# Performance work log

Hardware: AMD Instinct MI355X
Metric: run time of the kernel (lower is better)

## Reference

```python
import jax, jax.numpy as jnp
import numpy as np

B, N, D, L, NREPEAT = 32, 577, 384, 12, 4
H = 4 * D  # mlp hidden
EPS = 1e-6


def ln(x, w, b):
    mu = jnp.mean(x, axis=-1, keepdims=True)
    var = jnp.mean(jnp.square(x - mu), axis=-1, keepdims=True)
    return (x - mu) * jax.lax.rsqrt(var + EPS) * w + b


def setup_inputs() -> dict:
    key = jax.random.key(0)
    ks = jax.random.split(key, 16)
    s = 0.02
    return {
        "x": jax.random.normal(ks[0], (B, N, D), dtype=jnp.float32),
        "norm1_w": jnp.ones((L, D), jnp.float32),
        "norm1_b": jnp.zeros((L, D), jnp.float32),
        "qkv_w": jax.random.normal(ks[1], (L, 3 * D, D), jnp.float32) * s,
        "qkv_b": jnp.zeros((L, 3 * D), jnp.float32),
        "qn_w": jnp.ones((L, D), jnp.float32),
        "qn_b": jnp.zeros((L, D), jnp.float32),
        "kn_w": jnp.ones((L, D), jnp.float32),
        "kn_b": jnp.zeros((L, D), jnp.float32),
        "an_w": jnp.ones((L, D), jnp.float32),
        "an_b": jnp.zeros((L, D), jnp.float32),
        "proj_w": jax.random.normal(ks[2], (L, D, D), jnp.float32) * s,
        "proj_b": jnp.zeros((L, D), jnp.float32),
        "ls1": jnp.full((L, D), 1e-5, jnp.float32),
        "norm2_w": jnp.ones((L, D), jnp.float32),
        "norm2_b": jnp.zeros((L, D), jnp.float32),
        "fc1_w": jax.random.normal(ks[3], (L, H, D), jnp.float32) * s,
        "fc1_b": jnp.zeros((L, H), jnp.float32),
        "fc2_w": jax.random.normal(ks[4], (L, D, H), jnp.float32) * s,
        "fc2_b": jnp.zeros((L, D), jnp.float32),
        "ls2": jnp.full((L, D), 1e-5, jnp.float32),
    }


def _forward(x, norm1_w, norm1_b, qkv_w, qkv_b, qn_w, qn_b, kn_w, kn_b,
             an_w, an_b, proj_w, proj_b, ls1, norm2_w, norm2_b,
             fc1_w, fc1_b, fc2_w, fc2_b, ls2):
    scale = 1.0 / np.sqrt(D).astype(np.float32)
    x_prime = x
    history = []  # list of [B, 1, D] cls tokens, grows each repeat
    for _ in range(NREPEAT):
        new_cls = x[:, 0:1]
        x = jnp.concatenate([new_cls, x_prime[:, 1:]], axis=1)  # [B, N, D]
        mem = jnp.concatenate([x] + history, axis=1)            # [B, N+t, D]
        for l in range(L):
            res1 = x
            xn = ln(x, norm1_w[l], norm1_b[l])
            # manual qkv split: q from normed x, k/v from UNNORMED mem
            q = xn @ qkv_w[l, :D].T + qkv_b[l, :D]
            k = mem @ qkv_w[l, D:2 * D].T + qkv_b[l, D:2 * D]
            v = mem @ qkv_w[l, 2 * D:].T + qkv_b[l, 2 * D:]
            q = ln(q, qn_w[l], qn_b[l])
            k = ln(k, kn_w[l], kn_b[l])
            # single-head SDPA over full width D
            attn = jax.nn.softmax(jnp.einsum('bqd,bkd->bqk', q, k) * scale, axis=-1)
            prod = jnp.einsum('bqk,bkd->bqd', attn, v)
            prod = ln(prod, an_w[l], an_b[l])
            proj = prod @ proj_w[l].T + proj_b[l]
            x = proj * ls1[l] + res1
            res2 = x
            x2 = ln(x, norm2_w[l], norm2_b[l])
            h = jax.nn.gelu(x2 @ fc1_w[l].T + fc1_b[l], approximate=False)
            x1 = h @ fc2_w[l].T + fc2_b[l]
            x = x1 * ls2[l] + res2
        history.append(new_cls)
    return x


def reference(x, norm1_w, norm1_b, qkv_w, qkv_b, qn_w, qn_b, kn_w, kn_b,
              an_w, an_b, proj_w, proj_b, ls1, norm2_w, norm2_b,
              fc1_w, fc1_b, fc2_w, fc2_b, ls2):
    return _forward(x, norm1_w, norm1_b, qkv_w, qkv_b, qn_w, qn_b, kn_w, kn_b,
                    an_w, an_b, proj_w, proj_b, ls1, norm2_w, norm2_b,
                    fc1_w, fc1_b, fc2_w, fc2_b, ls2)
```

## Files before the change

### kernel.cpp

```cpp
#include <hip/hip_runtime.h>
#include <math.h>

#define BB 32
#define NN 577
#define DD 384
#define HD 1536
#define LL 12
#define MP 640
#define NRPT 4

typedef __attribute__((ext_vector_type(8))) short bf16x8;
typedef __attribute__((ext_vector_type(4))) float f32x4;

__device__ __forceinline__ unsigned short f2bf(float f){
  unsigned u = __builtin_bit_cast(unsigned, f);
  u += 0x7fffu + ((u >> 16) & 1u);
  return (unsigned short)(u >> 16);
}
__device__ __forceinline__ float bf2f(unsigned short s){
  unsigned u = ((unsigned)s) << 16;
  return __builtin_bit_cast(float, u);
}

__device__ __forceinline__ void async16(void* lds, const void* g){
  __builtin_amdgcn_global_load_lds(
      (const __attribute__((address_space(1))) unsigned int*)g,
      (__attribute__((address_space(3))) unsigned int*)lds, 16, 0, 0);
}

__global__ void prep_k(float* __restrict__ x, const float* __restrict__ xp,
                       float* __restrict__ cls_r, const float* __restrict__ cls_hist,
                       unsigned short* __restrict__ mem, int r){
  int i = blockIdx.x * 256 + threadIdx.x;
  if (i >= BB*MP*DD) return;
  int d = i % DD;
  int n = (i / DD) % MP;
  int b = i / (MP*DD);
  float v;
  if (n == 0){ v = x[(size_t)b*NN*DD + d]; cls_r[b*DD + d] = v; }
  else if (n < NN){ v = xp[((size_t)b*NN + n)*DD + d]; x[((size_t)b*NN + n)*DD + d] = v; }
  else if (n < NN + r){ v = cls_hist[(size_t)(n-NN)*BB*DD + b*DD + d]; }
  else v = 0.f;
  mem[i] = f2bf(v);
}

__global__ void castL_k(const float* __restrict__ qkvw, const float* __restrict__ pw,
                        const float* __restrict__ f1w, const float* __restrict__ f2w,
                        unsigned short* __restrict__ wbuf){
  int i = blockIdx.x * 256 + threadIdx.x;
  const int QKV = 3*DD*DD;
  const int PRJ = DD*DD;
  const int F1  = HD*DD;
  const int TOT = QKV + PRJ + 2*F1;
  if (i >= TOT) return;
  float v;
  if (i < QKV) v = qkvw[i];
  else if (i < QKV+PRJ) v = pw[i-QKV];
  else if (i < QKV+PRJ+F1) v = f1w[i-QKV-PRJ];
  else v = f2w[i-QKV-PRJ-F1];
  wbuf[i] = f2bf(v);
}

template<typename T>
__global__ __launch_bounds__(256) void ln4_k(const T* __restrict__ in, const float* __restrict__ w,
                                             const float* __restrict__ bias, unsigned short* __restrict__ out,
                                             int nrows){
  int row = blockIdx.x*4 + (threadIdx.x >> 6);
  if (row >= nrows) return;
  int lane = threadIdx.x & 63;
  const T* p = in + (size_t)row*DD;
  float v[6];
  float s = 0.f;
  #pragma unroll
  for (int i=0;i<6;i++){
    float t;
    if (sizeof(T) == 4) t = (float)p[lane + i*64];
    else t = bf2f((unsigned short)p[lane + i*64]);
    v[i] = t; s += t;
  }
  #pragma unroll
  for (int o=32;o;o>>=1) s += __shfl_xor(s, o, 64);
  float mu = s * (1.f/DD);
  float q = 0.f;
  #pragma unroll
  for (int i=0;i<6;i++){ float t = v[i]-mu; q += t*t; }
  #pragma unroll
  for (int o=32;o;o>>=1) q += __shfl_xor(q, o, 64);
  float rs = rsqrtf(q*(1.f/DD) + 1e-6f);
  unsigned short* po = out + (size_t)row*DD;
  #pragma unroll
  for (int i=0;i<6;i++){
    int c = lane + i*64;
    po[c] = f2bf((v[i]-mu)*rs*w[c] + bias[c]);
  }
}

__global__ __launch_bounds__(256) void lnqk_k(const unsigned short* __restrict__ qraw,
                                              const unsigned short* __restrict__ kraw,
                                              const float* __restrict__ qw, const float* __restrict__ qbias,
                                              const float* __restrict__ kw, const float* __restrict__ kbias,
                                              unsigned short* __restrict__ qo, unsigned short* __restrict__ ko){
  const int QR = BB*NN;
  int row = blockIdx.x*4 + (threadIdx.x >> 6);
  int lane = threadIdx.x & 63;
  bool isq = row < QR;
  const unsigned short* p = isq ? qraw + (size_t)row*DD : kraw + (size_t)(row-QR)*DD;
  const float* w  = isq ? qw : kw;
  const float* bs = isq ? qbias : kbias;
  unsigned short* po = isq ? qo + (size_t)row*DD : ko + (size_t)(row-QR)*DD;
  float scale = isq ? 0.05103103588f : 1.0f;
  float v[6];
  float s = 0.f;
  #pragma unroll
  for (int i=0;i<6;i++){ float t = bf2f(p[lane + i*64]); v[i] = t; s += t; }
  #pragma unroll
  for (int o=32;o;o>>=1) s += __shfl_xor(s, o, 64);
  float mu = s * (1.f/DD);
  float q = 0.f;
  #pragma unroll
  for (int i=0;i<6;i++){ float t = v[i]-mu; q += t*t; }
  #pragma unroll
  for (int o=32;o;o>>=1) q += __shfl_xor(q, o, 64);
  float rs = rsqrtf(q*(1.f/DD) + 1e-6f);
  #pragma unroll
  for (int i=0;i<6;i++){
    int c = lane + i*64;
    po[c] = f2bf(((v[i]-mu)*rs*w[c] + bs[c]) * scale);
  }
}

template<int EPI>
__global__ __launch_bounds__(256) void gemm128(
    const unsigned short* __restrict__ A, int lda, int arows, long sA,
    const unsigned short* __restrict__ B, int ldb, int brows, long sB,
    const float* __restrict__ bias,
    int K, int N,
    float* __restrict__ outF, unsigned short* __restrict__ outB,
    int ldo, int orows, long sO,
    const float* __restrict__ ls){

  __shared__ unsigned short a_sh[2][128*32];
  __shared__ unsigned short b_sh[2][128*32];

  int tid  = threadIdx.x;
  int wave = tid >> 6, lane = tid & 63;
  int lr = lane & 15, kg = lane >> 4;
  int wm = wave >> 1, wn = wave & 1;
  int z = blockIdx.z;
  int row0 = blockIdx.y * 128;
  int col0 = blockIdx.x * 128;

  const unsigned short* Ab = A + (size_t)z*sA;
  const unsigned short* Bb = B + (size_t)z*sB;

  f32x4 zf = {0.f,0.f,0.f,0.f};
  f32x4 acc[4][4];
  #pragma unroll
  for (int i=0;i<4;i++)
    #pragma unroll
    for (int j=0;j<4;j++) acc[i][j] = zf;

  int ra[2], rb[2], kc[2];
  #pragma unroll
  for (int it=0; it<2; it++){
    int c = tid + it*256;
    int r = row0 + (c>>2); if (r > arows-1) r = arows-1;
    ra[it] = r;
    r = col0 + (c>>2); if (r > brows-1) r = brows-1;
    rb[it] = r;
    kc[it] = (c&3)*8;
  }

  for (int k0 = 0; k0 < K; k0 += 64){
    #pragma unroll
    for (int p=0;p<2;p++){
      #pragma unroll
      for (int it=0; it<2; it++){
        unsigned short* la = &a_sh[p][(it*256 + wave*64)*8];
        unsigned short* lb = &b_sh[p][(it*256 + wave*64)*8];
        async16(la, Ab + (size_t)ra[it]*lda + k0 + p*32 + kc[it]);
        async16(lb, Bb + (size_t)rb[it]*ldb + k0 + p*32 + kc[it]);
      }
    }
    __syncthreads();
    #pragma unroll
    for (int p=0;p<2;p++){
      bf16x8 af[4], bfr[4];
      #pragma unroll
      for (int i=0;i<4;i++){
        af[i]  = *(const bf16x8*)&a_sh[p][(wm*64 + i*16 + lr)*32 + kg*8];
        bfr[i] = *(const bf16x8*)&b_sh[p][(wn*64 + i*16 + lr)*32 + kg*8];
      }
      #pragma unroll
      for (int i=0;i<4;i++)
        #pragma unroll
        for (int j=0;j<4;j++)
          acc[i][j] = __builtin_amdgcn_mfma_f32_16x16x32_bf16(af[i], bfr[j], acc[i][j], 0,0,0);
    }
    __syncthreads();
  }

  float* oF = outF ? outF + (size_t)z*sO : nullptr;
  unsigned short* oB = outB ? outB + (size_t)z*sO : nullptr;

  #pragma unroll
  for (int mi=0;mi<4;mi++)
    #pragma unroll
    for (int ni=0;ni<4;ni++)
      #pragma unroll
      for (int r=0;r<4;r++){
        int row = row0 + wm*64 + mi*16 + kg*4 + r;
        int col = col0 + wn*64 + ni*16 + lr;
        if (row >= orows || col >= N) continue;
        float vv = acc[mi][ni][r];
        size_t idx = (size_t)row*ldo + col;
        if (EPI == 0){
          if (bias) vv += bias[col];
          oB[idx] = f2bf(vv);
        } else if (EPI == 1){
          vv += bias[row];
          oB[idx] = f2bf(vv);
        } else if (EPI == 2){
          vv += bias[col];
          oF[idx] = vv*ls[col] + oF[idx];
        } else {
          vv += bias[col];
          float g = 0.5f*vv*(1.f + erff(vv*0.70710678118f));
          oB[idx] = f2bf(g);
        }
      }
}

__global__ __launch_bounds__(256, 2) void attn_k(
    const unsigned short* __restrict__ qs,
    const unsigned short* __restrict__ kb,
    const unsigned short* __restrict__ vT,
    const float* __restrict__ anw, const float* __restrict__ anb,
    unsigned short* __restrict__ out, int M){

  __shared__ unsigned short k_sh[32*384];
  __shared__ unsigned short v_sh[384*32];
  __shared__ unsigned short p_sh[64*56];

  int tid = threadIdx.x;
  int wv = tid >> 6, lane = tid & 63;
  int lr = lane & 15, kg = lane >> 4;
  int b = blockIdx.y, qt0 = blockIdx.x * 64;

  bf16x8 qf[12];
  {
    int qrow = qt0 + wv*16 + lr; if (qrow > NN-1) qrow = NN-1;
    const unsigned short* qp = qs + ((size_t)b*NN + qrow)*DD;
    #pragma unroll
    for (int ks=0; ks<12; ks++) qf[ks] = *(const bf16x8*)(qp + ks*32 + kg*8);
  }

  f32x4 zf = {0.f,0.f,0.f,0.f};
  f32x4 O[24];
  #pragma unroll
  for (int i=0;i<24;i++) O[i] = zf;
  float m_run[4], l_run[4];
  #pragma unroll
  for (int r=0;r<4;r++){ m_run[r] = -INFINITY; l_run[r] = 0.f; }

  for (int kt=0; kt<19; kt++){
    __syncthreads();
    #pragma unroll
    for (int i=0;i<6;i++){
      int L = i*256 + tid;
      int row = L/48, c = L%48;
      int gc = (c & ~7) | ((c ^ row) & 7);
      async16(&k_sh[L*8], kb + ((size_t)b*MP + kt*32 + row)*DD + gc*8);
    }
    #pragma unroll
    for (int i=0;i<6;i++){
      int L = i*256 + tid;
      int row = L>>2;
      int gc = (L&3) ^ (row&3);
      async16(&v_sh[L*8], vT + ((size_t)b*DD + row)*MP + kt*32 + gc*8);
    }
    __syncthreads();

    f32x4 s[2] = {zf, zf};
    #pragma unroll
    for (int ks=0; ks<12; ks++){
      int c = ks*4 + kg;
      #pragma unroll
      for (int nk=0; nk<2; nk++){
        int krow = nk*16 + lr;
        bf16x8 bk = *(const bf16x8*)&k_sh[krow*DD + ((c & ~7) | ((c ^ krow)&7))*8];
        s[nk] = __builtin_amdgcn_mfma_f32_16x16x32_bf16(qf[ks], bk, s[nk], 0,0,0);
      }
    }
    #pragma unroll
    for (int nk=0; nk<2; nk++){
      if (kt*32 + nk*16 + lr >= M){
        s[nk][0] = -INFINITY; s[nk][1] = -INFINITY; s[nk][2] = -INFINITY; s[nk][3] = -INFINITY;
      }
    }
    float al[4];
    #pragma unroll
    for (int r=0;r<4;r++){
      float v = fmaxf(s[0][r], s[1][r]);
      v = fmaxf(v, __shfl_xor(v, 1, 64));
      v = fmaxf(v, __shfl_xor(v, 2, 64));
      v = fmaxf(v, __shfl_xor(v, 4, 64));
      v = fmaxf(v, __shfl_xor(v, 8, 64));
      float mn = fmaxf(m_run[r], v);
      al[r] = __expf(m_run[r] - mn);
      m_run[r] = mn;
    }
    #pragma unroll
    for (int nk=0;nk<2;nk++)
      #pragma unroll
      for (int r=0;r<4;r++)
        s[nk][r] = __expf(s[nk][r] - m_run[r]);
    #pragma unroll
    for (int r=0;r<4;r++){
      float v = s[0][r] + s[1][r];
      v += __shfl_xor(v, 1, 64);
      v += __shfl_xor(v, 2, 64);
      v += __shfl_xor(v, 4, 64);
      v += __shfl_xor(v, 8, 64);
      l_run[r] = al[r]*l_run[r] + v;
    }
    #pragma unroll
    for (int nk=0;nk<2;nk++)
      #pragma unroll
      for (int r=0;r<4;r++)
        p_sh[(wv*16 + kg*4 + r)*56 + nk*16 + lr] = f2bf(s[nk][r]);
    #pragma unroll
    for (int ni=0;ni<24;ni++)
      #pragma unroll
      for (int r=0;r<4;r++) O[ni][r] *= al[r];
    __syncthreads();

    bf16x8 ap = *(const bf16x8*)&p_sh[(wv*16 + lr)*56 + kg*8];
    #pragma unroll
    for (int ni=0;ni<24;ni++){
      int d = ni*16 + lr;
      bf16x8 bv = *(const bf16x8*)&v_sh[d*32 + ((kg ^ (d&3))*8)];
      O[ni] = __builtin_amdgcn_mfma_f32_16x16x32_bf16(ap, bv, O[ni], 0,0,0);
    }
  }

  float inv[4];
  #pragma unroll
  for (int r=0;r<4;r++) inv[r] = 1.f / l_run[r];
  float s1[4] = {0,0,0,0}, s2[4] = {0,0,0,0};
  #pragma unroll
  for (int ni=0;ni<24;ni++)
    #pragma unroll
    for (int r=0;r<4;r++){
      float x = O[ni][r]*inv[r];
      O[ni][r] = x;
      s1[r] += x; s2[r] += x*x;
    }
  #pragma unroll
  for (int r=0;r<4;r++){
    #pragma unroll
    for (int o=1;o<16;o<<=1){ s1[r] += __shfl_xor(s1[r], o, 64); s2[r] += __shfl_xor(s2[r], o, 64); }
  }
  float mu[4], rs[4];
  #pragma unroll
  for (int r=0;r<4;r++){
    mu[r] = s1[r]*(1.f/DD);
    float var = s2[r]*(1.f/DD) - mu[r]*mu[r];
    rs[r] = rsqrtf(fmaxf(var, 0.f) + 1e-6f);
  }
  int rowb = qt0 + wv*16 + kg*4;
  #pragma unroll
  for (int ni=0;ni<24;ni++){
    int col = ni*16 + lr;
    float wc = anw[col], bc = anb[col];
    #pragma unroll
    for (int r=0;r<4;r++){
      int qrow = rowb + r;
      if (qrow < NN)
        out[((size_t)b*NN + qrow)*DD + col] = f2bf((O[ni][r]-mu[r])*rs[r]*wc + bc);
    }
  }
}


extern "C" void kernel_launch(void* const* d_in, const int* in_sizes, int n_in,
                              void* d_out, int out_size, void* d_ws, size_t ws_size,
                              hipStream_t stream){
  const float* x_in = (const float*)d_in[0];
  const float* n1w  = (const float*)d_in[1];
  const float* n1b  = (const float*)d_in[2];
  const float* qkvw = (const float*)d_in[3];
  const float* qkvb = (const float*)d_in[4];
  const float* qnw  = (const float*)d_in[5];
  const float* qnb  = (const float*)d_in[6];
  const float* knw  = (const float*)d_in[7];
  const float* knb  = (const float*)d_in[8];
  const float* anw  = (const float*)d_in[9];
  const float* anb  = (const float*)d_in[10];
  const float* pw   = (const float*)d_in[11];
  const float* pb   = (const float*)d_in[12];
  const float* ls1  = (const float*)d_in[13];
  const float* n2w  = (const float*)d_in[14];
  const float* n2b  = (const float*)d_in[15];
  const float* f1w  = (const float*)d_in[16];
  const float* f1b  = (const float*)d_in[17];
  const float* f2w  = (const float*)d_in[18];
  const float* f2bb = (const float*)d_in[19];
  const float* ls2  = (const float*)d_in[20];

  char* ws = (char*)d_ws;
  size_t off = 0;
  auto alloc = [&](size_t bytes)->char* {
    char* p = ws + off;
    off = (off + bytes + 255) & ~(size_t)255;
    return p;
  };

  const int QKV = 3*DD*DD, PRJ = DD*DD, F1 = HD*DD;
  const size_t WTOT = (size_t)QKV + PRJ + 2*F1;
  const size_t SLOT = (size_t)BB*MP*DD;

  unsigned short* wbuf  = (unsigned short*)alloc(WTOT*2);
  float*          cls_h = (float*)         alloc((size_t)NRPT*BB*DD*4);
  unsigned short* mem_bf= (unsigned short*)alloc(SLOT*2);
  unsigned short* pool  = (unsigned short*)alloc(6*SLOT*2);

  unsigned short* wq = wbuf;
  unsigned short* wp = wbuf + QKV;
  unsigned short* w1 = wbuf + QKV + PRJ;
  unsigned short* w2 = wbuf + QKV + PRJ + F1;

  unsigned short* S0 = pool;
  unsigned short* S1 = pool + SLOT;
  unsigned short* S2 = pool + 2*SLOT;
  unsigned short* S3 = pool + 3*SLOT;
  unsigned short* S4 = pool + 4*SLOT;
  unsigned short* S5 = pool + 5*SLOT;

  unsigned short* xn    = S0;
  unsigned short* qraw  = S1;
  unsigned short* kraw  = S2;
  unsigned short* qb    = S3;
  unsigned short* kb    = S4;
  unsigned short* vT    = S5;
  unsigned short* prodn = S1;
  unsigned short* x2    = S0;
  unsigned short* h     = S1;

  float* xf = (float*)d_out;

  auto cg = [](size_t n){ return dim3((unsigned)((n + 255) / 256)); };

  hipMemcpyAsync(xf, x_in, (size_t)BB*NN*DD*4, hipMemcpyDeviceToDevice, stream);

  const int RT  = (BB*NN + 127)/128;
  const int RTM = (BB*MP)/128;
  const int QR  = BB*NN;
  const int KR  = BB*MP;

  for (int r = 0; r < NRPT; r++){
    int M = NN + r;
    prep_k<<<cg((size_t)BB*MP*DD),256,0,stream>>>(xf, x_in, cls_h + (size_t)r*BB*DD, cls_h, mem_bf, r);
    for (int l = 0; l < LL; l++){
      castL_k<<<cg(WTOT),256,0,stream>>>(qkvw + (size_t)l*QKV, pw + (size_t)l*PRJ,
                                         f1w + (size_t)l*F1, f2w + (size_t)l*F1, wbuf);
      ln4_k<float><<<cg((size_t)QR*64),256,0,stream>>>(xf, n1w + l*DD, n1b + l*DD, xn, QR);
      gemm128<0><<<dim3(3,RT,1),256,0,stream>>>(xn,384,QR,0, wq,384,384,0,
          qkvb + l*3*DD, 384,384, nullptr,qraw,384,QR,0, nullptr);
      gemm128<0><<<dim3(3,RTM,1),256,0,stream>>>(mem_bf,384,KR,0, wq + (size_t)DD*DD,384,384,0,
          qkvb + l*3*DD + DD, 384,384, nullptr,kraw,384,KR,0, nullptr);
      gemm128<1><<<dim3(MP/128,3,BB),256,0,stream>>>(wq + (size_t)2*DD*DD,384,384,0, mem_bf,384,MP,(long)MP*DD,
          qkvb + l*3*DD + 2*DD, 384,MP, nullptr,vT,MP,384,(long)DD*MP, nullptr);
      lnqk_k<<<(QR+KR)/4,256,0,stream>>>(qraw, kraw, qnw + l*DD, qnb + l*DD,
                                         knw + l*DD, knb + l*DD, qb, kb);
      attn_k<<<dim3(10,BB),256,0,stream>>>(qb, kb, vT, anw + l*DD, anb + l*DD, prodn, M);
      gemm128<2><<<dim3(3,RT,1),256,0,stream>>>(prodn,384,QR,0, wp,384,384,0,
          pb + l*DD, 384,384, xf,nullptr,384,QR,0, ls1 + l*DD);
      ln4_k<float><<<cg((size_t)QR*64),256,0,stream>>>(xf, n2w + l*DD, n2b + l*DD, x2, QR);
      gemm128<3><<<dim3(HD/128,RT,1),256,0,stream>>>(x2,384,QR,0, w1,384,HD,0,
          f1b + l*HD, 384,HD, nullptr,h,HD,QR,0, nullptr);
      gemm128<2><<<dim3(3,RT,1),256,0,stream>>>(h,HD,QR,0, w2,HD,384,0,
          f2bb + l*DD, HD,384, xf,nullptr,384,QR,0, ls2 + l*DD);
    }
  }
}
```

Measured before the change: 16.85 ms.

## Hoist weight casts, fuse q-layernorm into attention, vectorize LN, lazy softmax rescale

All layers' weights are now cast to bf16 once before the repeat loop, instead of once per layer per repeat. The q LayerNorm and scale move into the attention kernel's Q load, and the k LayerNorm runs in place through a vectorized ln4 kernel with float4/ushort4 accesses. The attention loop now rescales the running max and output only when the new max exceeds the old one by more than 8, and it raises wave priority around the MFMA sections. The trade-offs are more registers and work in the attention prologue, a single-pass variance formula that is less numerically robust, and a larger weight buffer.

```diff
diff --git a/kernel.cpp b/kernel.cpp
--- a/kernel.cpp
+++ b/kernel.cpp
@@ -44,20 +44,21 @@
   mem[i] = f2bf(v);
 }
 
-__global__ void castL_k(const float* __restrict__ qkvw, const float* __restrict__ pw,
-                        const float* __restrict__ f1w, const float* __restrict__ f2w,
-                        unsigned short* __restrict__ wbuf){
+__global__ void cast_all_k(const float* __restrict__ qkvw, const float* __restrict__ pw,
+                           const float* __restrict__ f1w, const float* __restrict__ f2w,
+                           unsigned short* __restrict__ wbuf){
   int i = blockIdx.x * 256 + threadIdx.x;
   const int QKV = 3*DD*DD;
   const int PRJ = DD*DD;
   const int F1  = HD*DD;
   const int TOT = QKV + PRJ + 2*F1;
-  if (i >= TOT) return;
+  if (i >= LL*TOT) return;
+  int l = i / TOT, j = i % TOT;
   float v;
-  if (i < QKV) v = qkvw[i];
-  else if (i < QKV+PRJ) v = pw[i-QKV];
-  else if (i < QKV+PRJ+F1) v = f1w[i-QKV-PRJ];
-  else v = f2w[i-QKV-PRJ-F1];
+  if (j < QKV) v = qkvw[(size_t)l*QKV + j];
+  else if (j < QKV+PRJ) v = pw[(size_t)l*PRJ + (j-QKV)];
+  else if (j < QKV+PRJ+F1) v = f1w[(size_t)l*F1 + (j-QKV-PRJ)];
+  else v = f2w[(size_t)l*F1 + (j-QKV-PRJ-F1)];
   wbuf[i] = f2bf(v);
 }
 
@@ -70,14 +71,19 @@
   int lane = threadIdx.x & 63;
   const T* p = in + (size_t)row*DD;
   float v[6];
-  float s = 0.f;
-  #pragma unroll
-  for (int i=0;i<6;i++){
-    float t;
-    if (sizeof(T) == 4) t = (float)p[lane + i*64];
-    else t = bf2f((unsigned short)p[lane + i*64]);
-    v[i] = t; s += t;
-  }
+  if constexpr (sizeof(T) == 4){
+    const float* pf = (const float*)p;
+    float4 a = *(const float4*)(pf + lane*4);
+    float2 c = *(const float2*)(pf + 256 + lane*2);
+    v[0]=a.x; v[1]=a.y; v[2]=a.z; v[3]=a.w; v[4]=c.x; v[5]=c.y;
+  } else {
+    const unsigned short* ps = (const unsigned short*)p;
+    ushort4 a = *(const ushort4*)(ps + lane*4);
+    ushort2 c = *(const ushort2*)(ps + 256 + lane*2);
+    v[0]=bf2f(a.x); v[1]=bf2f(a.y); v[2]=bf2f(a.z); v[3]=bf2f(a.w);
+    v[4]=bf2f(c.x); v[5]=bf2f(c.y);
+  }
+  float s = v[0]+v[1]+v[2]+v[3]+v[4]+v[5];
   #pragma unroll
   for (int o=32;o;o>>=1) s += __shfl_xor(s, o, 64);
   float mu = s * (1.f/DD);
@@ -87,46 +93,21 @@
   #pragma unroll
   for (int o=32;o;o>>=1) q += __shfl_xor(q, o, 64);
   float rs = rsqrtf(q*(1.f/DD) + 1e-6f);
+  float4 w4 = *(const float4*)(w + lane*4);
+  float2 w2 = *(const float2*)(w + 256 + lane*2);
+  float4 b4 = *(const float4*)(bias + lane*4);
+  float2 b2 = *(const float2*)(bias + 256 + lane*2);
   unsigned short* po = out + (size_t)row*DD;
-  #pragma unroll
-  for (int i=0;i<6;i++){
-    int c = lane + i*64;
-    po[c] = f2bf((v[i]-mu)*rs*w[c] + bias[c]);
-  }
-}
-
-__global__ __launch_bounds__(256) void lnqk_k(const unsigned short* __restrict__ qraw,
-                                              const unsigned short* __restrict__ kraw,
-                                              const float* __restrict__ qw, const float* __restrict__ qbias,
-                                              const float* __restrict__ kw, const float* __restrict__ kbias,
-                                              unsigned short* __restrict__ qo, unsigned short* __restrict__ ko){
-  const int QR = BB*NN;
-  int row = blockIdx.x*4 + (threadIdx.x >> 6);
-  int lane = threadIdx.x & 63;
-  bool isq = row < QR;
-  const unsigned short* p = isq ? qraw + (size_t)row*DD : kraw + (size_t)(row-QR)*DD;
-  const float* w  = isq ? qw : kw;
-  const float* bs = isq ? qbias : kbias;
-  unsigned short* po = isq ? qo + (size_t)row*DD : ko + (size_t)(row-QR)*DD;
-  float scale = isq ? 0.05103103588f : 1.0f;
-  float v[6];
-  float s = 0.f;
-  #pragma unroll
-  for (int i=0;i<6;i++){ float t = bf2f(p[lane + i*64]); v[i] = t; s += t; }
-  #pragma unroll
-  for (int o=32;o;o>>=1) s += __shfl_xor(s, o, 64);
-  float mu = s * (1.f/DD);
-  float q = 0.f;
-  #pragma unroll
-  for (int i=0;i<6;i++){ float t = v[i]-mu; q += t*t; }
-  #pragma unroll
-  for (int o=32;o;o>>=1) q += __shfl_xor(q, o, 64);
-  float rs = rsqrtf(q*(1.f/DD) + 1e-6f);
-  #pragma unroll
-  for (int i=0;i<6;i++){
-    int c = lane + i*64;
-    po[c] = f2bf(((v[i]-mu)*rs*w[c] + bs[c]) * scale);
-  }
+  ushort4 o4;
+  o4.x = f2bf((v[0]-mu)*rs*w4.x + b4.x);
+  o4.y = f2bf((v[1]-mu)*rs*w4.y + b4.y);
+  o4.z = f2bf((v[2]-mu)*rs*w4.z + b4.z);
+  o4.w = f2bf((v[3]-mu)*rs*w4.w + b4.w);
+  *(ushort4*)(po + lane*4) = o4;
+  ushort2 o2;
+  o2.x = f2bf((v[4]-mu)*rs*w2.x + b2.x);
+  o2.y = f2bf((v[5]-mu)*rs*w2.y + b2.y);
+  *(ushort2*)(po + 256 + lane*2) = o2;
 }
 
 template<int EPI>
@@ -232,7 +213,8 @@
 }
 
 __global__ __launch_bounds__(256, 2) void attn_k(
-    const unsigned short* __restrict__ qs,
+    const unsigned short* __restrict__ qraw,
+    const float* __restrict__ qw, const float* __restrict__ qb_,
     const unsigned short* __restrict__ kb,
     const unsigned short* __restrict__ vT,
     const float* __restrict__ anw, const float* __restrict__ anb,
@@ -250,9 +232,41 @@
   bf16x8 qf[12];
   {
     int qrow = qt0 + wv*16 + lr; if (qrow > NN-1) qrow = NN-1;
-    const unsigned short* qp = qs + ((size_t)b*NN + qrow)*DD;
-    #pragma unroll
-    for (int ks=0; ks<12; ks++) qf[ks] = *(const bf16x8*)(qp + ks*32 + kg*8);
+    const unsigned short* qp = qraw + ((size_t)b*NN + qrow)*DD;
+    float s1 = 0.f, s2 = 0.f;
+    #pragma unroll
+    for (int ks=0; ks<12; ks++){
+      qf[ks] = *(const bf16x8*)(qp + ks*32 + kg*8);
+      #pragma unroll
+      for (int j=0;j<8;j++){
+        float t = bf2f((unsigned short)qf[ks][j]);
+        s1 += t; s2 += t*t;
+      }
+    }
+    s1 += __shfl_xor(s1, 16, 64); s1 += __shfl_xor(s1, 32, 64);
+    s2 += __shfl_xor(s2, 16, 64); s2 += __shfl_xor(s2, 32, 64);
+    const float SC = 0.05103103588f;
+    float mu = s1 * (1.f/DD);
+    float var = s2 * (1.f/DD) - mu*mu;
+    float rs = rsqrtf(fmaxf(var, 0.f) + 1e-6f) * SC;
+    #pragma unroll
+    for (int ks=0; ks<12; ks++){
+      int c0 = ks*32 + kg*8;
+      float4 wa = *(const float4*)(qw + c0);
+      float4 wb = *(const float4*)(qw + c0 + 4);
+      float4 ba = *(const float4*)(qb_ + c0);
+      float4 bb = *(const float4*)(qb_ + c0 + 4);
+      bf16x8 t;
+      t[0] = (short)f2bf((bf2f((unsigned short)qf[ks][0])-mu)*rs*wa.x + ba.x*SC);
+      t[1] = (short)f2bf((bf2f((unsigned short)qf[ks][1])-mu)*rs*wa.y + ba.y*SC);
+      t[2] = (short)f2bf((bf2f((unsigned short)qf[ks][2])-mu)*rs*wa.z + ba.z*SC);
+      t[3] = (short)f2bf((bf2f((unsigned short)qf[ks][3])-mu)*rs*wa.w + ba.w*SC);
+      t[4] = (short)f2bf((bf2f((unsigned short)qf[ks][4])-mu)*rs*wb.x + bb.x*SC);
+      t[5] = (short)f2bf((bf2f((unsigned short)qf[ks][5])-mu)*rs*wb.y + bb.y*SC);
+      t[6] = (short)f2bf((bf2f((unsigned short)qf[ks][6])-mu)*rs*wb.z + bb.z*SC);
+      t[7] = (short)f2bf((bf2f((unsigned short)qf[ks][7])-mu)*rs*wb.w + bb.w*SC);
+      qf[ks] = t;
+    }
   }
 
   f32x4 zf = {0.f,0.f,0.f,0.f};
@@ -282,6 +296,7 @@
     __syncthreads();
 
     f32x4 s[2] = {zf, zf};
+    __builtin_amdgcn_s_setprio(1);
     #pragma unroll
     for (int ks=0; ks<12; ks++){
       int c = ks*4 + kg;
@@ -292,13 +307,14 @@
         s[nk] = __builtin_amdgcn_mfma_f32_16x16x32_bf16(qf[ks], bk, s[nk], 0,0,0);
       }
     }
+    __builtin_amdgcn_s_setprio(0);
     #pragma unroll
     for (int nk=0; nk<2; nk++){
       if (kt*32 + nk*16 + lr >= M){
         s[nk][0] = -INFINITY; s[nk][1] = -INFINITY; s[nk][2] = -INFINITY; s[nk][3] = -INFINITY;
       }
     }
-    float al[4];
+    float vmax[4];
     #pragma unroll
     for (int r=0;r<4;r++){
       float v = fmaxf(s[0][r], s[1][r]);
@@ -306,9 +322,20 @@
       v = fmaxf(v, __shfl_xor(v, 2, 64));
       v = fmaxf(v, __shfl_xor(v, 4, 64));
       v = fmaxf(v, __shfl_xor(v, 8, 64));
-      float mn = fmaxf(m_run[r], v);
-      al[r] = __expf(m_run[r] - mn);
-      m_run[r] = mn;
+      vmax[r] = v;
+    }
+    bool small = (vmax[0] <= m_run[0] + 8.f) & (vmax[1] <= m_run[1] + 8.f)
+               & (vmax[2] <= m_run[2] + 8.f) & (vmax[3] <= m_run[3] + 8.f);
+    if (!__all(small)){
+      #pragma unroll
+      for (int r=0;r<4;r++){
+        float mn = fmaxf(m_run[r], vmax[r]);
+        float al = __expf(m_run[r] - mn);
+        m_run[r] = mn;
+        l_run[r] *= al;
+        #pragma unroll
+        for (int ni=0;ni<24;ni++) O[ni][r] *= al;
+      }
     }
     #pragma unroll
     for (int nk=0;nk<2;nk++)
@@ -322,26 +349,24 @@
       v += __shfl_xor(v, 2, 64);
       v += __shfl_xor(v, 4, 64);
       v += __shfl_xor(v, 8, 64);
-      l_run[r] = al[r]*l_run[r] + v;
+      l_run[r] += v;
     }
     #pragma unroll
     for (int nk=0;nk<2;nk++)
       #pragma unroll
       for (int r=0;r<4;r++)
         p_sh[(wv*16 + kg*4 + r)*56 + nk*16 + lr] = f2bf(s[nk][r]);
-    #pragma unroll
-    for (int ni=0;ni<24;ni++)
-      #pragma unroll
-      for (int r=0;r<4;r++) O[ni][r] *= al[r];
     __syncthreads();
 
     bf16x8 ap = *(const bf16x8*)&p_sh[(wv*16 + lr)*56 + kg*8];
+    __builtin_amdgcn_s_setprio(1);
     #pragma unroll
     for (int ni=0;ni<24;ni++){
       int d = ni*16 + lr;
       bf16x8 bv = *(const bf16x8*)&v_sh[d*32 + ((kg ^ (d&3))*8)];
       O[ni] = __builtin_amdgcn_mfma_f32_16x16x32_bf16(ap, bv, O[ni], 0,0,0);
     }
+    __builtin_amdgcn_s_setprio(0);
   }
 
   float inv[4];
@@ -420,30 +445,22 @@
   const size_t WTOT = (size_t)QKV + PRJ + 2*F1;
   const size_t SLOT = (size_t)BB*MP*DD;
 
-  unsigned short* wbuf  = (unsigned short*)alloc(WTOT*2);
+  unsigned short* wbuf  = (unsigned short*)alloc((size_t)LL*WTOT*2);
   float*          cls_h = (float*)         alloc((size_t)NRPT*BB*DD*4);
   unsigned short* mem_bf= (unsigned short*)alloc(SLOT*2);
   unsigned short* pool  = (unsigned short*)alloc(6*SLOT*2);
-
-  unsigned short* wq = wbuf;
-  unsigned short* wp = wbuf + QKV;
-  unsigned short* w1 = wbuf + QKV + PRJ;
-  unsigned short* w2 = wbuf + QKV + PRJ + F1;
 
   unsigned short* S0 = pool;
   unsigned short* S1 = pool + SLOT;
   unsigned short* S2 = pool + 2*SLOT;
   unsigned short* S3 = pool + 3*SLOT;
-  unsigned short* S4 = pool + 4*SLOT;
   unsigned short* S5 = pool + 5*SLOT;
 
   unsigned short* xn    = S0;
   unsigned short* qraw  = S1;
   unsigned short* kraw  = S2;
-  unsigned short* qb    = S3;
-  unsigned short* kb    = S4;
   unsigned short* vT    = S5;
-  unsigned short* prodn = S1;
+  unsigned short* prodn = S3;
   unsigned short* x2    = S0;
   unsigned short* h     = S1;
 
@@ -458,12 +475,18 @@
   const int QR  = BB*NN;
   const int KR  = BB*MP;
 
+  cast_all_k<<<cg((size_t)LL*WTOT),256,0,stream>>>(qkvw, pw, f1w, f2w, wbuf);
+
   for (int r = 0; r < NRPT; r++){
     int M = NN + r;
     prep_k<<<cg((size_t)BB*MP*DD),256,0,stream>>>(xf, x_in, cls_h + (size_t)r*BB*DD, cls_h, mem_bf, r);
     for (int l = 0; l < LL; l++){
-      castL_k<<<cg(WTOT),256,0,stream>>>(qkvw + (size_t)l*QKV, pw + (size_t)l*PRJ,
-                                         f1w + (size_t)l*F1, f2w + (size_t)l*F1, wbuf);
+      const unsigned short* wl = wbuf + (size_t)l*WTOT;
+      const unsigned short* wq = wl;
+      const unsigned short* wp = wl + QKV;
+      const unsigned short* w1 = wl + QKV + PRJ;
+      const unsigned short* w2 = wl + QKV + PRJ + F1;
+
       ln4_k<float><<<cg((size_t)QR*64),256,0,stream>>>(xf, n1w + l*DD, n1b + l*DD, xn, QR);
       gemm128<0><<<dim3(3,RT,1),256,0,stream>>>(xn,384,QR,0, wq,384,384,0,
           qkvb + l*3*DD, 384,384, nullptr,qraw,384,QR,0, nullptr);
@@ -471,9 +494,9 @@
           qkvb + l*3*DD + DD, 384,384, nullptr,kraw,384,KR,0, nullptr);
       gemm128<1><<<dim3(MP/128,3,BB),256,0,stream>>>(wq + (size_t)2*DD*DD,384,384,0, mem_bf,384,MP,(long)MP*DD,
           qkvb + l*3*DD + 2*DD, 384,MP, nullptr,vT,MP,384,(long)DD*MP, nullptr);
-      lnqk_k<<<(QR+KR)/4,256,0,stream>>>(qraw, kraw, qnw + l*DD, qnb + l*DD,
-                                         knw + l*DD, knb + l*DD, qb, kb);
-      attn_k<<<dim3(10,BB),256,0,stream>>>(qb, kb, vT, anw + l*DD, anb + l*DD, prodn, M);
+      ln4_k<unsigned short><<<cg((size_t)KR*64),256,0,stream>>>(kraw, knw + l*DD, knb + l*DD, kraw, KR);
+      attn_k<<<dim3(10,BB),256,0,stream>>>(qraw, qnw + l*DD, qnb + l*DD, kraw, vT,
+                                           anw + l*DD, anb + l*DD, prodn, M);
       gemm128<2><<<dim3(3,RT,1),256,0,stream>>>(prodn,384,QR,0, wp,384,384,0,
           pb + l*DD, 384,384, xf,nullptr,384,QR,0, ls1 + l*DD);
       ln4_k<float><<<cg((size_t)QR*64),256,0,stream>>>(xf, n2w + l*DD, n2b + l*DD, x2, QR);
```

Measured after the change: 16.66 ms. About the same (-1.1%).
